# Kernel optimization log

Measured on AMD Instinct MI355X. Metric: run time of the kernel, lower is better.

Reference implementation:

```python
import jax, jax.numpy as jnp
import numpy as np

L, K, H = 8192, 30, 128
SCALE = 30.0
LN_EPS = 1e-5


def _ln(x, g, b):
    mu = jnp.mean(x, axis=-1, keepdims=True)
    var = jnp.mean((x - mu) ** 2, axis=-1, keepdims=True)
    return (x - mu) * jax.lax.rsqrt(var + LN_EPS) * g + b


def _gelu(x):
    return jax.nn.gelu(x, approximate=False)  # torch.nn.GELU default (exact)


def setup_inputs() -> dict:
    key = jax.random.key(0)
    ks = jax.random.split(key, 16)

    def lin(k, din, dout):
        k1, k2 = jax.random.split(k)
        w = jax.random.normal(k1, (din, dout), jnp.float32) / np.sqrt(din).astype(np.float32)
        b = jax.random.normal(k2, (dout,), jnp.float32) * 0.01
        return w, b

    inp = {}
    inp['h_V'] = jax.random.normal(ks[0], (L, H), jnp.float32)
    inp['h_E'] = jax.random.normal(ks[1], (L, K, H), jnp.float32)
    inp['E_idx'] = jax.random.randint(ks[2], (L, K), 0, L, jnp.int32)
    inp['mask_V'] = jnp.ones((L,), jnp.float32)
    inp['mask_attend'] = jnp.ones((L, K), jnp.float32)

    D_in = 3 * H  # num_hidden + num_in = 128 + 256
    inp['W1'], inp['b1'] = lin(ks[3], D_in, H)
    inp['W2'], inp['b2'] = lin(ks[4], H, H)
    inp['W3'], inp['b3'] = lin(ks[5], H, H)
    inp['W11'], inp['b11'] = lin(ks[6], D_in, H)
    inp['W12'], inp['b12'] = lin(ks[7], H, H)
    inp['W13'], inp['b13'] = lin(ks[8], H, H)
    inp['Wi'], inp['bi'] = lin(ks[9], H, 4 * H)   # PositionWiseFeedForward.W_in
    inp['Wo'], inp['bo'] = lin(ks[10], 4 * H, H)  # PositionWiseFeedForward.W_out
    inp['g1'] = jnp.ones((H,), jnp.float32); inp['be1'] = jnp.zeros((H,), jnp.float32)
    inp['g2'] = jnp.ones((H,), jnp.float32); inp['be2'] = jnp.zeros((H,), jnp.float32)
    inp['g3'] = jnp.ones((H,), jnp.float32); inp['be3'] = jnp.zeros((H,), jnp.float32)
    return inp


def _forward(h_V, h_E, E_idx, mask_V, mask_attend,
             W1, b1, W2, b2, W3, b3, W11, b11, W12, b12, W13, b13,
             Wi, bi, Wo, bo, g1, be1, g2, be2, g3, be3):
    # --- node update: gather neighbors, concat, 3-layer MLP message, masked sum ---
    h_nb = h_V[E_idx]                                   # [L,K,H] gather_nodes
    h_EV = jnp.concatenate(
        [jnp.broadcast_to(h_V[:, None, :], (L, K, H)), h_E, h_nb], axis=-1)  # [L,K,3H]
    m = _gelu(h_EV @ W1 + b1)
    m = _gelu(m @ W2 + b2)
    m = m @ W3 + b3                                     # [L,K,H]
    m = mask_attend[..., None] * m
    dh = jnp.sum(m, axis=-2) / SCALE                    # [L,H]
    h_V = _ln(h_V + dh, g1, be1)
    # --- position-wise FFN ---
    dh = _gelu(h_V @ Wi + bi) @ Wo + bo
    h_V = _ln(h_V + dh, g2, be2)
    h_V = mask_V[:, None] * h_V
    # --- edge update ---
    h_nb = h_V[E_idx]
    h_EV = jnp.concatenate(
        [jnp.broadcast_to(h_V[:, None, :], (L, K, H)), h_E, h_nb], axis=-1)
    m = _gelu(h_EV @ W11 + b11)
    m = _gelu(m @ W12 + b12)
    m = m @ W13 + b13
    h_E = _ln(h_E + m, g3, be3)
    return h_V, h_E


def reference(h_V, h_E, E_idx, mask_V, mask_attend,
              W1, b1, W2, b2, W3, b3, W11, b11, W12, b12, W13, b13,
              Wi, bi, Wo, bo, g1, be1, g2, be2, g3, be3):
    return _forward(h_V, h_E, E_idx, mask_V, mask_attend,
                    W1, b1, W2, b2, W3, b3, W11, b11, W12, b12, W13, b13,
                    Wi, bi, Wo, bo, g1, be1, g2, be2, g3, be3)
```

## Files before the change

### kernel.cpp

```cpp
#include <hip/hip_runtime.h>
#include <math.h>

typedef unsigned short u16;
typedef __bf16 bf16x8 __attribute__((ext_vector_type(8)));
typedef float f32x4 __attribute__((ext_vector_type(4)));
typedef u16 u16x8 __attribute__((ext_vector_type(8)));

#define LTOT 8192
#define KNB  30
#define HDIM 128

__device__ __forceinline__ float bf2f(u16 u){
  unsigned x = ((unsigned)u) << 16;
  return __builtin_bit_cast(float, x);
}
__device__ __forceinline__ u16 f2bf(float f){
  __bf16 h = (__bf16)f;
  return __builtin_bit_cast(u16, h);
}
__device__ __forceinline__ float fast_exp2(float x){
#if __has_builtin(__builtin_amdgcn_exp2f)
  return __builtin_amdgcn_exp2f(x);
#else
  return exp2f(x);
#endif
}
__device__ __forceinline__ float gelu_f(float x){
  float x2 = x * x;
  float g  = x * (2.3022082f + 0.10294324f * x2);
  float e  = fast_exp2(g);
  float r  = __builtin_amdgcn_rcpf(e + 1.f);
  return x * (1.f - r);
}
__device__ __forceinline__ void pack8(u16* dst, const float* s){
  float4 a = *(const float4*)s, b = *(const float4*)(s + 4);
  u16x8 p;
  p[0]=f2bf(a.x); p[1]=f2bf(a.y); p[2]=f2bf(a.z); p[3]=f2bf(a.w);
  p[4]=f2bf(b.x); p[5]=f2bf(b.y); p[6]=f2bf(b.z); p[7]=f2bf(b.w);
  *(u16x8*)dst = p;
}

struct TEnt { const float* src; u16* dst; int K; int N; int nb; };
struct TTab { TEnt e[12]; };

__global__ __launch_bounds__(256) void transpose_kernel(TTab t){
  int b = (int)blockIdx.x;
  for (int i = 0; i < 12; ++i){
    int nb = t.e[i].nb;
    if (b < nb){
      int N = t.e[i].N, Kd = t.e[i].K;
      int idx = b * 256 + (int)threadIdx.x;
      if (idx < Kd * N){
        int k = idx / N;
        int n = idx - k * N;
        t.e[i].dst[n * Kd + k] = f2bf(t.e[i].src[(long)k * N + n]);
      }
      return;
    }
    b -= nb;
  }
}

__global__ __launch_bounds__(256) void pre_gemm_kernel(
  const float* __restrict__ X,
  const u16* __restrict__ WTa, const float* __restrict__ ba, u16* __restrict__ outa,
  const u16* __restrict__ WTc, u16* __restrict__ outc)
{
  __shared__ __align__(16) char smem[8704];
  u16* Xs = (u16*)smem;
  const int tid = threadIdx.x;
  const int wave = tid >> 6, lane = tid & 63, q = lane >> 4, s = lane & 15;
  const int w = (int)blockIdx.x & 1;
  const int row0 = ((int)blockIdx.x >> 1) * 32;

  for (int i = tid; i < 32 * 16; i += 256){
    int r = i >> 4, cb = i & 15;
    pack8(&Xs[r * 136 + cb * 8], &X[(long)(row0 + r) * HDIM + cb * 8]);
  }
  __syncthreads();
  const u16* W = w ? WTc : WTa;
  u16* out = w ? outc : outa;
  f32x4 acc[2][2];
#pragma unroll
  for (int mt = 0; mt < 2; ++mt)
#pragma unroll
    for (int nt = 0; nt < 2; ++nt){ f32x4 z = {0.f,0.f,0.f,0.f}; acc[mt][nt] = z; }
  for (int kt = 0; kt < 4; ++kt){
    bf16x8 b0 = *(const bf16x8*)&W[(wave * 32 + s) * 128 + kt * 32 + q * 8];
    bf16x8 b1 = *(const bf16x8*)&W[(wave * 32 + 16 + s) * 128 + kt * 32 + q * 8];
#pragma unroll
    for (int mt = 0; mt < 2; ++mt){
      bf16x8 af = *(const bf16x8*)&Xs[(mt * 16 + s) * 136 + kt * 32 + q * 8];
      acc[mt][0] = __builtin_amdgcn_mfma_f32_16x16x32_bf16(af, b0, acc[mt][0], 0, 0, 0);
      acc[mt][1] = __builtin_amdgcn_mfma_f32_16x16x32_bf16(af, b1, acc[mt][1], 0, 0, 0);
    }
  }
#pragma unroll
  for (int nt = 0; nt < 2; ++nt){
    int col = wave * 32 + nt * 16 + s;
    float bv = w ? 0.f : ba[col];
#pragma unroll
    for (int mt = 0; mt < 2; ++mt)
#pragma unroll
      for (int r = 0; r < 4; ++r){
        int row = row0 + mt * 16 + q * 4 + r;
        out[(long)row * HDIM + col] = f2bf(acc[mt][nt][r] + bv);
      }
  }
}

template<bool EDGE>
__global__ __launch_bounds__(256, 4) void msg_kernel(
  const float* __restrict__ hVin,
  const float* __restrict__ hE,
  const int* __restrict__ Eidx,
  const float* __restrict__ maskA,
  const u16* __restrict__ vsum,
  const u16* __restrict__ vcg,
  const u16* __restrict__ WTb, const u16* __restrict__ WT2, const u16* __restrict__ WT3,
  const float* __restrict__ b2, const float* __restrict__ b3,
  const float* __restrict__ gam, const float* __restrict__ bet,
  float* __restrict__ out_f32,
  u16* __restrict__ out_b16,
  float* __restrict__ outE)
{
  __shared__ __align__(16) char smem[36096];
  u16*   As   = (u16*)smem;
  float* ovl  = (float*)smem;
  u16*   Vs   = (u16*)(smem + 17408);
  float* vbuf = (float*)(smem + 34816);
  float* mbuf = (float*)(smem + 35840);

  const int tid = threadIdx.x;
  const int wave = tid >> 6, lane = tid & 63, q = lane >> 4, s = lane & 15;
  const int node0 = (int)blockIdx.x * 2;

  const int r0 = tid >> 4, cbch = tid & 15;
  int ed[4];
#pragma unroll
  for (int j = 0; j < 4; ++j){
    int r = r0 + j * 16;
    int nd = r >> 5, k = r & 31;
    ed[j] = (k < KNB) ? Eidx[(node0 + nd) * KNB + k] : 0;
  }
#pragma unroll
  for (int j = 0; j < 4; ++j){
    int r = r0 + j * 16;
    *(u16x8*)&Vs[r * 136 + cbch * 8] = *(const u16x8*)&vcg[(long)ed[j] * HDIM + cbch * 8];
  }
#pragma unroll
  for (int j = 0; j < 4; ++j){
    int r = r0 + j * 16;
    int nd = r >> 5, k = r & 31;
    if (k < KNB)
      pack8(&As[r * 136 + cbch * 8], &hE[(((long)(node0 + nd) * KNB) + k) * HDIM + cbch * 8]);
    else { u16x8 z = {0,0,0,0,0,0,0,0}; *(u16x8*)&As[r * 136 + cbch * 8] = z; }
  }
  if (!EDGE && tid < 64){
    int nd = tid >> 5, k = tid & 31;
    mbuf[tid] = (k < KNB) ? maskA[(node0 + nd) * KNB + k] : 0.f;
  }
  vbuf[tid] = bf2f(vsum[(long)(node0 + (tid >> 7)) * HDIM + (tid & 127)]);
  float hv0 = 0.f, hv1 = 0.f;
  if (!EDGE && wave < 2){
    hv0 = hVin[(long)(node0 + wave) * HDIM + lane];
    hv1 = hVin[(long)(node0 + wave) * HDIM + 64 + lane];
  }

  f32x4 acc[4][2];
  for (int layer = 0; layer < 3; ++layer){
    const u16* W = (layer == 0) ? WTb : ((layer == 1) ? WT2 : WT3);
    __syncthreads();
#pragma unroll
    for (int mt = 0; mt < 4; ++mt){ f32x4 z = {0.f,0.f,0.f,0.f}; acc[mt][0] = z; acc[mt][1] = z; }
    for (int kt = 0; kt < 4; ++kt){
      bf16x8 b0 = *(const bf16x8*)&W[(wave * 32 + s) * 128 + kt * 32 + q * 8];
      bf16x8 b1 = *(const bf16x8*)&W[(wave * 32 + 16 + s) * 128 + kt * 32 + q * 8];
#pragma unroll
      for (int mt = 0; mt < 4; ++mt){
        bf16x8 af = *(const bf16x8*)&As[(mt * 16 + s) * 136 + kt * 32 + q * 8];
        acc[mt][0] = __builtin_amdgcn_mfma_f32_16x16x32_bf16(af, b0, acc[mt][0], 0, 0, 0);
        acc[mt][1] = __builtin_amdgcn_mfma_f32_16x16x32_bf16(af, b1, acc[mt][1], 0, 0, 0);
      }
    }
    if (layer < 2){
      __syncthreads();
#pragma unroll
      for (int nt = 0; nt < 2; ++nt){
        int col = wave * 32 + nt * 16 + s;
        float bv = (layer == 1) ? b2[col] : 0.f;
        float vb0 = 0.f, vb1 = 0.f;
        if (layer == 0){ vb0 = vbuf[col]; vb1 = vbuf[128 + col]; }
#pragma unroll
        for (int mt = 0; mt < 4; ++mt)
#pragma unroll
          for (int r = 0; r < 4; ++r){
            int row = mt * 16 + q * 4 + r;
            float v = acc[mt][nt][r] + bv;
            if (layer == 0)
              v += (mt < 2 ? vb0 : vb1) + bf2f(Vs[row * 136 + col]);
            As[row * 136 + col] = f2bf(gelu_f(v));
          }
      }
    }
  }

  if (EDGE){
#pragma unroll
    for (int nt = 0; nt < 2; ++nt){
      int col = wave * 32 + nt * 16 + s;
      float b3v = b3[col];
#pragma unroll
      for (int mt = 0; mt < 4; ++mt)
#pragma unroll
        for (int r = 0; r < 4; ++r){
          int row = mt * 16 + q * 4 + r, nd = row >> 5, k = row & 31;
          float z = acc[mt][nt][r] + b3v;
          if (k < KNB) z += hE[(((long)(node0 + nd) * KNB) + k) * HDIM + col];
          acc[mt][nt][r] = z;
        }
    }
  }
  __syncthreads();

  if (!EDGE){
    float* dh = ovl;
#pragma unroll
    for (int nt = 0; nt < 2; ++nt){
      int col = wave * 32 + nt * 16 + s;
      float b3v = b3[col];
#pragma unroll
      for (int ni = 0; ni < 2; ++ni){
        float ss = 0.f;
#pragma unroll
        for (int mh = 0; mh < 2; ++mh){
          int mt = ni * 2 + mh;
#pragma unroll
          for (int r = 0; r < 4; ++r){
            int row = mt * 16 + q * 4 + r;
            ss += (acc[mt][nt][r] + b3v) * mbuf[row];
          }
        }
        ss += __shfl_xor(ss, 16);
        ss += __shfl_xor(ss, 32);
        if (q == 0) dh[ni * 128 + col] = ss * (1.f / 30.f);
      }
    }
    __syncthreads();
    if (wave < 2){
      int node = node0 + wave;
      float x0 = hv0 + dh[wave * 128 + lane];
      float x1 = hv1 + dh[wave * 128 + 64 + lane];
      float sm = x0 + x1, s2 = x0 * x0 + x1 * x1;
#pragma unroll
      for (int o = 32; o; o >>= 1){ sm += __shfl_xor(sm, o); s2 += __shfl_xor(s2, o); }
      float mu = sm * (1.f / 128.f);
      float var = fmaxf(s2 * (1.f / 128.f) - mu * mu, 0.f);
      float rs = rsqrtf(var + 1e-5f);
      float y0 = (x0 - mu) * rs * gam[lane]      + bet[lane];
      float y1 = (x1 - mu) * rs * gam[64 + lane] + bet[64 + lane];
      out_f32[(long)node * HDIM + lane]      = y0;
      out_f32[(long)node * HDIM + 64 + lane] = y1;
      out_b16[(long)node * HDIM + lane]      = f2bf(y0);
      out_b16[(long)node * HDIM + 64 + lane] = f2bf(y1);
    }
  } else {
    float* part  = ovl;
    float* part2 = ovl + 256;
    float* muv   = ovl + 512;
    float* rsv   = ovl + 576;
#pragma unroll
    for (int mt = 0; mt < 4; ++mt)
#pragma unroll
      for (int r = 0; r < 4; ++r){
        int row = mt * 16 + q * 4 + r;
        float ps = acc[mt][0][r] + acc[mt][1][r];
        float pq = acc[mt][0][r] * acc[mt][0][r] + acc[mt][1][r] * acc[mt][1][r];
#pragma unroll
        for (int o = 1; o < 16; o <<= 1){ ps += __shfl_xor(ps, o); pq += __shfl_xor(pq, o); }
        if (s == 0){ part[row * 4 + wave] = ps; part2[row * 4 + wave] = pq; }
      }
    __syncthreads();
    if (tid < 64){
      float sm = part[tid*4] + part[tid*4+1] + part[tid*4+2] + part[tid*4+3];
      float sq = part2[tid*4] + part2[tid*4+1] + part2[tid*4+2] + part2[tid*4+3];
      float mu = sm * (1.f / 128.f);
      float var = fmaxf(sq * (1.f / 128.f) - mu * mu, 0.f);
      muv[tid] = mu;
      rsv[tid] = rsqrtf(var + 1e-5f);
    }
    __syncthreads();
#pragma unroll
    for (int nt = 0; nt < 2; ++nt){
      int col = wave * 32 + nt * 16 + s;
      float gv = gam[col], bv = bet[col];
#pragma unroll
      for (int mt = 0; mt < 4; ++mt)
#pragma unroll
        for (int r = 0; r < 4; ++r){
          int row = mt * 16 + q * 4 + r, nd = row >> 5, k = row & 31;
          if (k < KNB){
            float y = (acc[mt][nt][r] - muv[row]) * rsv[row] * gv + bv;
            outE[(((long)(node0 + nd) * KNB) + k) * HDIM + col] = y;
          }
        }
    }
  }
}

__global__ __launch_bounds__(256) void ffn_kernel(
  const u16* __restrict__ xb, const float* __restrict__ xf,
  const u16* __restrict__ WiT,
  const u16* __restrict__ WoT,
  const float* __restrict__ bi, const float* __restrict__ bo,
  const float* __restrict__ g2, const float* __restrict__ be2,
  const float* __restrict__ maskV,
  const u16* __restrict__ W11aT, const float* __restrict__ b11,
  const u16* __restrict__ W11cT,
  float* __restrict__ outV, u16* __restrict__ vsum11, u16* __restrict__ vc2)
{
  __shared__ __align__(16) char smem[13696];
  u16*   Xs = (u16*)smem;
  u16*   Ts = (u16*)(smem + 4352);
  u16*   Ys = (u16*)(smem + 8704);
  float* part  = (float*)(smem + 13056);
  float* part2 = part + 64;
  float* muv   = part + 128;
  float* rsv   = part + 144;
  const int tid = threadIdx.x;
  const int wave = tid >> 6, lane = tid & 63, q = lane >> 4, s = lane & 15;
  const int row0 = (int)blockIdx.x * 16;

  float resid[2][4];
#pragma unroll
  for (int nt = 0; nt < 2; ++nt)
#pragma unroll
    for (int r = 0; r < 4; ++r)
      resid[nt][r] = xf[(long)(row0 + q * 4 + r) * HDIM + wave * 32 + nt * 16 + s];

  {
    int r = tid >> 4, cb = tid & 15;
    *(u16x8*)&Xs[r * 136 + cb * 8] = *(const u16x8*)&xb[(long)(row0 + r) * HDIM + cb * 8];
  }
  f32x4 yac[2];
  { f32x4 z = {0.f,0.f,0.f,0.f}; yac[0] = z; yac[1] = z; }

  for (int j = 0; j < 4; ++j){
    __syncthreads();
    f32x4 tac[2];
    { f32x4 z = {0.f,0.f,0.f,0.f}; tac[0] = z; tac[1] = z; }
    for (int kt = 0; kt < 4; ++kt){
      bf16x8 b0 = *(const bf16x8*)&WiT[((long)(j * 128 + wave * 32 + s)) * 128 + kt * 32 + q * 8];
      bf16x8 b1 = *(const bf16x8*)&WiT[((long)(j * 128 + wave * 32 + 16 + s)) * 128 + kt * 32 + q * 8];
      bf16x8 af = *(const bf16x8*)&Xs[s * 136 + kt * 32 + q * 8];
      tac[0] = __builtin_amdgcn_mfma_f32_16x16x32_bf16(af, b0, tac[0], 0, 0, 0);
      tac[1] = __builtin_amdgcn_mfma_f32_16x16x32_bf16(af, b1, tac[1], 0, 0, 0);
    }
#pragma unroll
    for (int nt = 0; nt < 2; ++nt){
      int col = wave * 32 + nt * 16 + s;
      float bv = bi[j * 128 + col];
#pragma unroll
      for (int r = 0; r < 4; ++r){
        int row = q * 4 + r;
        Ts[row * 136 + col] = f2bf(gelu_f(tac[nt][r] + bv));
      }
    }
    __syncthreads();
    for (int kt = 0; kt < 4; ++kt){
      bf16x8 b0 = *(const bf16x8*)&WoT[((long)(wave * 32 + s)) * 512 + j * 128 + kt * 32 + q * 8];
      bf16x8 b1 = *(const bf16x8*)&WoT[((long)(wave * 32 + 16 + s)) * 512 + j * 128 + kt * 32 + q * 8];
      bf16x8 af = *(const bf16x8*)&Ts[s * 136 + kt * 32 + q * 8];
      yac[0] = __builtin_amdgcn_mfma_f32_16x16x32_bf16(af, b0, yac[0], 0, 0, 0);
      yac[1] = __builtin_amdgcn_mfma_f32_16x16x32_bf16(af, b1, yac[1], 0, 0, 0);
    }
  }
#pragma unroll
  for (int nt = 0; nt < 2; ++nt){
    int col = wave * 32 + nt * 16 + s;
    float bv = bo[col];
#pragma unroll
    for (int r = 0; r < 4; ++r)
      yac[nt][r] += bv + resid[nt][r];
  }
#pragma unroll
  for (int r = 0; r < 4; ++r){
    int row = q * 4 + r;
    float ps = yac[0][r] + yac[1][r];
    float pq = yac[0][r] * yac[0][r] + yac[1][r] * yac[1][r];
#pragma unroll
    for (int o = 1; o < 16; o <<= 1){ ps += __shfl_xor(ps, o); pq += __shfl_xor(pq, o); }
    if (s == 0){ part[row * 4 + wave] = ps; part2[row * 4 + wave] = pq; }
  }
  __syncthreads();
  if (tid < 16){
    float sm = part[tid*4] + part[tid*4+1] + part[tid*4+2] + part[tid*4+3];
    float sq = part2[tid*4] + part2[tid*4+1] + part2[tid*4+2] + part2[tid*4+3];
    float mu = sm * (1.f / 128.f);
    float var = fmaxf(sq * (1.f / 128.f) - mu * mu, 0.f);
    muv[tid] = mu;
    rsv[tid] = rsqrtf(var + 1e-5f);
  }
  __syncthreads();
#pragma unroll
  for (int nt = 0; nt < 2; ++nt){
    int col = wave * 32 + nt * 16 + s;
    float gv = g2[col], bv = be2[col];
#pragma unroll
    for (int r = 0; r < 4; ++r){
      int row = q * 4 + r;
      float y = (yac[nt][r] - muv[row]) * rsv[row] * gv + bv;
      y *= maskV[row0 + row];
      outV[(long)(row0 + row) * HDIM + col] = y;
      Ys[row * 136 + col] = f2bf(y);
    }
  }
  __syncthreads();
  for (int w = 0; w < 2; ++w){
    const u16* W = w ? W11cT : W11aT;
    u16* out = w ? vc2 : vsum11;
    f32x4 acc[2];
    { f32x4 z = {0.f,0.f,0.f,0.f}; acc[0] = z; acc[1] = z; }
    for (int kt = 0; kt < 4; ++kt){
      bf16x8 b0 = *(const bf16x8*)&W[(wave * 32 + s) * 128 + kt * 32 + q * 8];
      bf16x8 b1 = *(const bf16x8*)&W[(wave * 32 + 16 + s) * 128 + kt * 32 + q * 8];
      bf16x8 af = *(const bf16x8*)&Ys[s * 136 + kt * 32 + q * 8];
      acc[0] = __builtin_amdgcn_mfma_f32_16x16x32_bf16(af, b0, acc[0], 0, 0, 0);
      acc[1] = __builtin_amdgcn_mfma_f32_16x16x32_bf16(af, b1, acc[1], 0, 0, 0);
    }
#pragma unroll
    for (int nt = 0; nt < 2; ++nt){
      int col = wave * 32 + nt * 16 + s;
      float bv = w ? 0.f : b11[col];
#pragma unroll
      for (int r = 0; r < 4; ++r){
        int row = row0 + q * 4 + r;
        out[(long)row * HDIM + col] = f2bf(acc[nt][r] + bv);
      }
    }
  }
}

extern "C" void kernel_launch(void* const* d_in, const int* in_sizes, int n_in,
                              void* d_out, int out_size, void* d_ws, size_t ws_size,
                              hipStream_t stream) {
  const float* hV    = (const float*)d_in[0];
  const float* hE    = (const float*)d_in[1];
  const int*   Eidx  = (const int*)d_in[2];
  const float* maskV = (const float*)d_in[3];
  const float* maskA = (const float*)d_in[4];
  const float* W1  = (const float*)d_in[5];  const float* b1  = (const float*)d_in[6];
  const float* W2  = (const float*)d_in[7];  const float* b2  = (const float*)d_in[8];
  const float* W3  = (const float*)d_in[9];  const float* b3  = (const float*)d_in[10];
  const float* W11 = (const float*)d_in[11]; const float* b11 = (const float*)d_in[12];
  const float* W12 = (const float*)d_in[13]; const float* b12 = (const float*)d_in[14];
  const float* W13 = (const float*)d_in[15]; const float* b13 = (const float*)d_in[16];
  const float* Wi  = (const float*)d_in[17]; const float* bi  = (const float*)d_in[18];
  const float* Wo  = (const float*)d_in[19]; const float* bo  = (const float*)d_in[20];
  const float* g1  = (const float*)d_in[21]; const float* be1 = (const float*)d_in[22];
  const float* g2  = (const float*)d_in[23]; const float* be2 = (const float*)d_in[24];
  const float* g3  = (const float*)d_in[25]; const float* be3 = (const float*)d_in[26];

  char* ws = (char*)d_ws;
  u16* wt = (u16*)ws;
  u16* wtW1a  = wt;
  u16* wtW1b  = wt + 16384;
  u16* wtW1c  = wt + 32768;
  u16* wtW2   = wt + 49152;
  u16* wtW3   = wt + 65536;
  u16* wtW11a = wt + 81920;
  u16* wtW11b = wt + 98304;
  u16* wtW11c = wt + 114688;
  u16* wtW12  = wt + 131072;
  u16* wtW13  = wt + 147456;
  u16* wtWi   = wt + 163840;
  u16* wtWo   = wt + 229376;
  size_t off = 589824;
  u16* vsum1   = (u16*)(ws + off); off += 2097152;
  u16* vc      = (u16*)(ws + off); off += 2097152;
  u16* vsum11  = (u16*)(ws + off); off += 2097152;
  u16* vc2     = (u16*)(ws + off); off += 2097152;
  float* hv1_f32 = (float*)(ws + off); off += 4194304;
  u16*   hv1_b16 = (u16*)(ws + off);   off += 2097152;

  float* outV = (float*)d_out;
  float* outE = (float*)d_out + (long)LTOT * HDIM;

  TTab tt;
  tt.e[0]  = { W1,          wtW1a,  128, 128, 64 };
  tt.e[1]  = { W1 + 16384,  wtW1b,  128, 128, 64 };
  tt.e[2]  = { W1 + 32768,  wtW1c,  128, 128, 64 };
  tt.e[3]  = { W2,          wtW2,   128, 128, 64 };
  tt.e[4]  = { W3,          wtW3,   128, 128, 64 };
  tt.e[5]  = { W11,         wtW11a, 128, 128, 64 };
  tt.e[6]  = { W11 + 16384, wtW11b, 128, 128, 64 };
  tt.e[7]  = { W11 + 32768, wtW11c, 128, 128, 64 };
  tt.e[8]  = { W12,         wtW12,  128, 128, 64 };
  tt.e[9]  = { W13,         wtW13,  128, 128, 64 };
  tt.e[10] = { Wi,          wtWi,   128, 512, 256 };
  tt.e[11] = { Wo,          wtWo,   512, 128, 256 };
  transpose_kernel<<<dim3(1152), dim3(256), 0, stream>>>(tt);

  pre_gemm_kernel<<<dim3(512), dim3(256), 0, stream>>>(
      hV, wtW1a, b1, vsum1, wtW1c, vc);
  msg_kernel<false><<<dim3(4096), dim3(256), 0, stream>>>(
      hV, hE, Eidx, maskA, vsum1, vc, wtW1b, wtW2, wtW3, b2, b3, g1, be1,
      hv1_f32, hv1_b16, nullptr);
  ffn_kernel<<<dim3(512), dim3(256), 0, stream>>>(
      hv1_b16, hv1_f32, wtWi, wtWo, bi, bo, g2, be2, maskV,
      wtW11a, b11, wtW11c, outV, vsum11, vc2);
  msg_kernel<true><<<dim3(4096), dim3(256), 0, stream>>>(
      hV, hE, Eidx, maskA, vsum11, vc2, wtW11b, wtW12, wtW13, b12, b13, g3, be3,
      hv1_f32, hv1_b16, outE);
}
```

Before: 444.0 us.

## Process four nodes per block with eight waves each owning a 16-column slice

The message kernel now handles four nodes (128 edge rows) per 512-thread block instead of two nodes per 256-thread block. Each of the eight waves owns 16 output columns across all 128 rows, so each weight fragment is loaded once and reused over eight M-tiles. LDS use doubles to about 72 KB, which can lower the number of blocks resident per CU. The LayerNorm partial reductions are reworked to combine eight waves.

```diff
diff --git a/kernel.cpp b/kernel.cpp
--- a/kernel.cpp
+++ b/kernel.cpp
@@ -110,7 +110,7 @@
 }
 
 template<bool EDGE>
-__global__ __launch_bounds__(256, 4) void msg_kernel(
+__global__ __launch_bounds__(512, 4) void msg_kernel(
   const float* __restrict__ hVin,
   const float* __restrict__ hE,
   const int* __restrict__ Eidx,
@@ -124,130 +124,111 @@
   u16* __restrict__ out_b16,
   float* __restrict__ outE)
 {
-  __shared__ __align__(16) char smem[36096];
+  __shared__ __align__(16) char smem[72192];
   u16*   As   = (u16*)smem;
   float* ovl  = (float*)smem;
-  u16*   Vs   = (u16*)(smem + 17408);
-  float* vbuf = (float*)(smem + 34816);
-  float* mbuf = (float*)(smem + 35840);
+  u16*   Vs   = (u16*)(smem + 34816);
+  float* vbuf = (float*)(smem + 69632);
+  float* mbuf = (float*)(smem + 71680);
 
   const int tid = threadIdx.x;
   const int wave = tid >> 6, lane = tid & 63, q = lane >> 4, s = lane & 15;
-  const int node0 = (int)blockIdx.x * 2;
-
-  const int r0 = tid >> 4, cbch = tid & 15;
+  const int node0 = (int)blockIdx.x * 4;
+
+  const int r0 = tid >> 4, cb = tid & 15;
   int ed[4];
 #pragma unroll
+  for (int j = 0; j < 4; ++j)
+    ed[j] = (r0 < KNB) ? Eidx[(node0 + j) * KNB + r0] : 0;
+#pragma unroll
   for (int j = 0; j < 4; ++j){
-    int r = r0 + j * 16;
-    int nd = r >> 5, k = r & 31;
-    ed[j] = (k < KNB) ? Eidx[(node0 + nd) * KNB + k] : 0;
+    int r = r0 + j * 32;
+    *(u16x8*)&Vs[r * 136 + cb * 8] = *(const u16x8*)&vcg[(long)ed[j] * HDIM + cb * 8];
   }
 #pragma unroll
   for (int j = 0; j < 4; ++j){
-    int r = r0 + j * 16;
-    *(u16x8*)&Vs[r * 136 + cbch * 8] = *(const u16x8*)&vcg[(long)ed[j] * HDIM + cbch * 8];
-  }
-#pragma unroll
-  for (int j = 0; j < 4; ++j){
-    int r = r0 + j * 16;
-    int nd = r >> 5, k = r & 31;
-    if (k < KNB)
-      pack8(&As[r * 136 + cbch * 8], &hE[(((long)(node0 + nd) * KNB) + k) * HDIM + cbch * 8]);
-    else { u16x8 z = {0,0,0,0,0,0,0,0}; *(u16x8*)&As[r * 136 + cbch * 8] = z; }
-  }
-  if (!EDGE && tid < 64){
+    int r = r0 + j * 32;
+    if (r0 < KNB)
+      pack8(&As[r * 136 + cb * 8], &hE[(((long)(node0 + j) * KNB) + r0) * HDIM + cb * 8]);
+    else { u16x8 z = {0,0,0,0,0,0,0,0}; *(u16x8*)&As[r * 136 + cb * 8] = z; }
+  }
+  if (!EDGE && tid < 128){
     int nd = tid >> 5, k = tid & 31;
     mbuf[tid] = (k < KNB) ? maskA[(node0 + nd) * KNB + k] : 0.f;
   }
   vbuf[tid] = bf2f(vsum[(long)(node0 + (tid >> 7)) * HDIM + (tid & 127)]);
   float hv0 = 0.f, hv1 = 0.f;
-  if (!EDGE && wave < 2){
+  if (!EDGE && wave < 4){
     hv0 = hVin[(long)(node0 + wave) * HDIM + lane];
     hv1 = hVin[(long)(node0 + wave) * HDIM + 64 + lane];
   }
 
-  f32x4 acc[4][2];
+  const int col = wave * 16 + s;
+  f32x4 acc[8];
   for (int layer = 0; layer < 3; ++layer){
     const u16* W = (layer == 0) ? WTb : ((layer == 1) ? WT2 : WT3);
     __syncthreads();
 #pragma unroll
-    for (int mt = 0; mt < 4; ++mt){ f32x4 z = {0.f,0.f,0.f,0.f}; acc[mt][0] = z; acc[mt][1] = z; }
+    for (int mt = 0; mt < 8; ++mt){ f32x4 z = {0.f,0.f,0.f,0.f}; acc[mt] = z; }
     for (int kt = 0; kt < 4; ++kt){
-      bf16x8 b0 = *(const bf16x8*)&W[(wave * 32 + s) * 128 + kt * 32 + q * 8];
-      bf16x8 b1 = *(const bf16x8*)&W[(wave * 32 + 16 + s) * 128 + kt * 32 + q * 8];
-#pragma unroll
-      for (int mt = 0; mt < 4; ++mt){
+      bf16x8 b0 = *(const bf16x8*)&W[col * 128 + kt * 32 + q * 8];
+#pragma unroll
+      for (int mt = 0; mt < 8; ++mt){
         bf16x8 af = *(const bf16x8*)&As[(mt * 16 + s) * 136 + kt * 32 + q * 8];
-        acc[mt][0] = __builtin_amdgcn_mfma_f32_16x16x32_bf16(af, b0, acc[mt][0], 0, 0, 0);
-        acc[mt][1] = __builtin_amdgcn_mfma_f32_16x16x32_bf16(af, b1, acc[mt][1], 0, 0, 0);
+        acc[mt] = __builtin_amdgcn_mfma_f32_16x16x32_bf16(af, b0, acc[mt], 0, 0, 0);
       }
     }
     if (layer < 2){
       __syncthreads();
-#pragma unroll
-      for (int nt = 0; nt < 2; ++nt){
-        int col = wave * 32 + nt * 16 + s;
-        float bv = (layer == 1) ? b2[col] : 0.f;
-        float vb0 = 0.f, vb1 = 0.f;
-        if (layer == 0){ vb0 = vbuf[col]; vb1 = vbuf[128 + col]; }
-#pragma unroll
-        for (int mt = 0; mt < 4; ++mt)
-#pragma unroll
-          for (int r = 0; r < 4; ++r){
-            int row = mt * 16 + q * 4 + r;
-            float v = acc[mt][nt][r] + bv;
-            if (layer == 0)
-              v += (mt < 2 ? vb0 : vb1) + bf2f(Vs[row * 136 + col]);
-            As[row * 136 + col] = f2bf(gelu_f(v));
-          }
-      }
+      float bv = (layer == 1) ? b2[col] : 0.f;
+#pragma unroll
+      for (int mt = 0; mt < 8; ++mt)
+#pragma unroll
+        for (int r = 0; r < 4; ++r){
+          int row = mt * 16 + q * 4 + r;
+          float v = acc[mt][r] + bv;
+          if (layer == 0)
+            v += vbuf[((row >> 5) << 7) + col] + bf2f(Vs[row * 136 + col]);
+          As[row * 136 + col] = f2bf(gelu_f(v));
+        }
     }
   }
 
   if (EDGE){
-#pragma unroll
-    for (int nt = 0; nt < 2; ++nt){
-      int col = wave * 32 + nt * 16 + s;
-      float b3v = b3[col];
-#pragma unroll
-      for (int mt = 0; mt < 4; ++mt)
-#pragma unroll
-        for (int r = 0; r < 4; ++r){
-          int row = mt * 16 + q * 4 + r, nd = row >> 5, k = row & 31;
-          float z = acc[mt][nt][r] + b3v;
-          if (k < KNB) z += hE[(((long)(node0 + nd) * KNB) + k) * HDIM + col];
-          acc[mt][nt][r] = z;
-        }
-    }
+    float b3v = b3[col];
+#pragma unroll
+    for (int mt = 0; mt < 8; ++mt)
+#pragma unroll
+      for (int r = 0; r < 4; ++r){
+        int row = mt * 16 + q * 4 + r, nd = row >> 5, k = row & 31;
+        float z = acc[mt][r] + b3v;
+        if (k < KNB) z += hE[(((long)(node0 + nd) * KNB) + k) * HDIM + col];
+        acc[mt][r] = z;
+      }
   }
   __syncthreads();
 
   if (!EDGE){
     float* dh = ovl;
-#pragma unroll
-    for (int nt = 0; nt < 2; ++nt){
-      int col = wave * 32 + nt * 16 + s;
-      float b3v = b3[col];
-#pragma unroll
-      for (int ni = 0; ni < 2; ++ni){
-        float ss = 0.f;
-#pragma unroll
-        for (int mh = 0; mh < 2; ++mh){
-          int mt = ni * 2 + mh;
-#pragma unroll
-          for (int r = 0; r < 4; ++r){
-            int row = mt * 16 + q * 4 + r;
-            ss += (acc[mt][nt][r] + b3v) * mbuf[row];
-          }
+    float b3v = b3[col];
+#pragma unroll
+    for (int nd = 0; nd < 4; ++nd){
+      float ss = 0.f;
+#pragma unroll
+      for (int mh = 0; mh < 2; ++mh){
+        int mt = nd * 2 + mh;
+#pragma unroll
+        for (int r = 0; r < 4; ++r){
+          int row = mt * 16 + q * 4 + r;
+          ss += (acc[mt][r] + b3v) * mbuf[row];
         }
-        ss += __shfl_xor(ss, 16);
-        ss += __shfl_xor(ss, 32);
-        if (q == 0) dh[ni * 128 + col] = ss * (1.f / 30.f);
-      }
-    }
-    __syncthreads();
-    if (wave < 2){
+      }
+      ss += __shfl_xor(ss, 16);
+      ss += __shfl_xor(ss, 32);
+      if (q == 0) dh[nd * 128 + col] = ss * (1.f / 30.f);
+    }
+    __syncthreads();
+    if (wave < 4){
       int node = node0 + wave;
       float x0 = hv0 + dh[wave * 128 + lane];
       float x1 = hv1 + dh[wave * 128 + 64 + lane];
@@ -266,45 +247,42 @@
     }
   } else {
     float* part  = ovl;
-    float* part2 = ovl + 256;
-    float* muv   = ovl + 512;
-    float* rsv   = ovl + 576;
-#pragma unroll
-    for (int mt = 0; mt < 4; ++mt)
+    float* part2 = ovl + 1024;
+    float* muv   = ovl + 2048;
+    float* rsv   = ovl + 2176;
+#pragma unroll
+    for (int mt = 0; mt < 8; ++mt)
 #pragma unroll
       for (int r = 0; r < 4; ++r){
         int row = mt * 16 + q * 4 + r;
-        float ps = acc[mt][0][r] + acc[mt][1][r];
-        float pq = acc[mt][0][r] * acc[mt][0][r] + acc[mt][1][r] * acc[mt][1][r];
+        float ps = acc[mt][r];
+        float pq = ps * ps;
 #pragma unroll
         for (int o = 1; o < 16; o <<= 1){ ps += __shfl_xor(ps, o); pq += __shfl_xor(pq, o); }
-        if (s == 0){ part[row * 4 + wave] = ps; part2[row * 4 + wave] = pq; }
-      }
-    __syncthreads();
-    if (tid < 64){
-      float sm = part[tid*4] + part[tid*4+1] + part[tid*4+2] + part[tid*4+3];
-      float sq = part2[tid*4] + part2[tid*4+1] + part2[tid*4+2] + part2[tid*4+3];
+        if (s == 0){ part[wave * 128 + row] = ps; part2[wave * 128 + row] = pq; }
+      }
+    __syncthreads();
+    if (tid < 128){
+      float sm = 0.f, sq = 0.f;
+#pragma unroll
+      for (int w2 = 0; w2 < 8; ++w2){ sm += part[w2 * 128 + tid]; sq += part2[w2 * 128 + tid]; }
       float mu = sm * (1.f / 128.f);
       float var = fmaxf(sq * (1.f / 128.f) - mu * mu, 0.f);
       muv[tid] = mu;
       rsv[tid] = rsqrtf(var + 1e-5f);
     }
     __syncthreads();
-#pragma unroll
-    for (int nt = 0; nt < 2; ++nt){
-      int col = wave * 32 + nt * 16 + s;
-      float gv = gam[col], bv = bet[col];
-#pragma unroll
-      for (int mt = 0; mt < 4; ++mt)
-#pragma unroll
-        for (int r = 0; r < 4; ++r){
-          int row = mt * 16 + q * 4 + r, nd = row >> 5, k = row & 31;
-          if (k < KNB){
-            float y = (acc[mt][nt][r] - muv[row]) * rsv[row] * gv + bv;
-            outE[(((long)(node0 + nd) * KNB) + k) * HDIM + col] = y;
-          }
+    float gv = gam[col], bv = bet[col];
+#pragma unroll
+    for (int mt = 0; mt < 8; ++mt)
+#pragma unroll
+      for (int r = 0; r < 4; ++r){
+        int row = mt * 16 + q * 4 + r, nd = row >> 5, k = row & 31;
+        if (k < KNB){
+          float y = (acc[mt][r] - muv[row]) * rsv[row] * gv + bv;
+          outE[(((long)(node0 + nd) * KNB) + k) * HDIM + col] = y;
         }
-    }
+      }
   }
 }
 
@@ -503,13 +481,13 @@
 
   pre_gemm_kernel<<<dim3(512), dim3(256), 0, stream>>>(
       hV, wtW1a, b1, vsum1, wtW1c, vc);
-  msg_kernel<false><<<dim3(4096), dim3(256), 0, stream>>>(
+  msg_kernel<false><<<dim3(2048), dim3(512), 0, stream>>>(
       hV, hE, Eidx, maskA, vsum1, vc, wtW1b, wtW2, wtW3, b2, b3, g1, be1,
       hv1_f32, hv1_b16, nullptr);
   ffn_kernel<<<dim3(512), dim3(256), 0, stream>>>(
       hv1_b16, hv1_f32, wtWi, wtWo, bi, bo, g2, be2, maskV,
       wtW11a, b11, wtW11c, outV, vsum11, vc2);
-  msg_kernel<true><<<dim3(4096), dim3(256), 0, stream>>>(
+  msg_kernel<true><<<dim3(2048), dim3(512), 0, stream>>>(
       hV, hE, Eidx, maskA, vsum11, vc2, wtW11b, wtW12, wtW13, b12, b13, g3, be3,
       hv1_f32, hv1_b16, outE);
 }
```

Measured after the change: 448.6 us. No clear change (+1.0%).
